# Performance work log

Measured on AMD Instinct MI355X. Metric: run time of the kernel, lower is better.

The kernel has to match this reference:

```python
import jax, jax.numpy as jnp
import numpy as np

INPUT_DIM = 256
EMBED_DIM = 256
NUM_HEADS = 8
HEAD_DIM = EMBED_DIM // NUM_HEADS
N_TOKENS = 11136
N_BATCH = 16


def _xavier(key, shape):
    fan_out, fan_in = shape
    bound = np.sqrt(6.0 / (fan_in + fan_out)).astype(np.float32)
    return jax.random.uniform(key, shape, jnp.float32, -bound, bound)


def setup_inputs() -> dict:
    key = jax.random.key(0)
    k_x, k_ids, k_qkv, k_o = jax.random.split(key, 4)
    x = jax.random.normal(k_x, (N_TOKENS, INPUT_DIM), jnp.float32)
    batch_ids = jnp.sort(jax.random.randint(k_ids, (N_TOKENS,), 0, N_BATCH)).astype(jnp.int32)
    qkv_w = _xavier(k_qkv, (3 * EMBED_DIM, INPUT_DIM))
    qkv_b = jnp.zeros((3 * EMBED_DIM,), jnp.float32)
    o_w = _xavier(k_o, (EMBED_DIM, EMBED_DIM))
    o_b = jnp.zeros((EMBED_DIM,), jnp.float32)
    return {"x": x, "batch_ids": batch_ids, "qkv_w": qkv_w, "qkv_b": qkv_b,
            "o_w": o_w, "o_b": o_b}


def reference(x, batch_ids, qkv_w, qkv_b, o_w, o_b):
    # batch_ids is concrete metadata (mirrors np.unique on CPU in the original).
    ids = np.asarray(batch_ids)
    vals, counts = np.unique(ids, return_counts=True)
    B = len(vals)
    S = int(counts.max())
    offsets = np.concatenate([np.zeros(1, np.int64), np.cumsum(counts)[:-1]])
    seg = np.searchsorted(vals, ids)               # segment index per token
    pos = np.arange(ids.shape[0]) - offsets[seg]   # position within segment

    qkv = x @ qkv_w.T + qkv_b                      # [N, 3E]
    # pad_sequence with padding_value=1 -> scatter tokens into an all-ones buffer
    fin = jnp.ones((B, S, 3 * EMBED_DIM), qkv.dtype).at[seg, pos].set(qkv)
    # padded rows sum to exactly 3E (all ones) -> mask True marks padding
    pad_mask = fin.sum(-1) >= fin.shape[-1]        # [B, S]

    qkv4 = fin.reshape(B, S, NUM_HEADS, 3 * HEAD_DIM).transpose(0, 2, 1, 3)
    q, k, v = jnp.split(qkv4, 3, axis=-1)          # each [B, H, S, hd]

    logits = jnp.einsum('bhqd,bhkd->bhqk', q, k) * (HEAD_DIM ** -0.5)
    logits = jnp.where(pad_mask[:, None, None, :], -jnp.inf, logits)
    attn = jax.nn.softmax(logits, axis=-1)         # [B, H, S, S]

    out = jnp.einsum('bhqk,bhkd->bhqd', attn, v)
    out = out.transpose(0, 2, 1, 3).reshape(B, S, EMBED_DIM)
    out = out[seg, pos]                            # unpad -> [N, E]
    return out @ o_w.T + o_b
```

## Files before the change

kernel.cpp:

```cpp
#include <hip/hip_runtime.h>
#include <stdint.h>


#define N_TOK 11136
#define E 256
#define H 8
#define HD 32

typedef __attribute__((ext_vector_type(8))) __bf16 bf16x8;
typedef __attribute__((ext_vector_type(8))) unsigned short u16x8;
typedef __attribute__((ext_vector_type(4))) float f32x4;

__device__ __forceinline__ unsigned short f2bf(float f) {
  unsigned int u = __float_as_uint(f);
  u = (u + 0x7FFFu + ((u >> 16) & 1u)) >> 16;
  return (unsigned short)u;
}
__device__ __forceinline__ float bf2f(unsigned short s) {
  return __uint_as_float(((unsigned int)s) << 16);
}
__device__ __forceinline__ bf16x8 ld8(const unsigned short* p) {
  return *(const bf16x8*)p;
}
__device__ __forceinline__ unsigned int cvtpk(float a, float b) {
  unsigned int r;
  asm("v_cvt_pk_bf16_f32 %0, %1, %2" : "=v"(r) : "v"(a), "v"(b));
  return r;
}

__global__ void k_split(const float* __restrict__ x, const float* __restrict__ qw,
                        const float* __restrict__ ow, const int* __restrict__ ids,
                        unsigned short* __restrict__ xhi, unsigned short* __restrict__ xlo,
                        unsigned short* __restrict__ whi, unsigned short* __restrict__ wlo,
                        unsigned short* __restrict__ owb, int* __restrict__ offs) {
  if (blockIdx.x == 0 && threadIdx.x < 17) {
    int b = threadIdx.x, lo = 0, hi = N_TOK;
    while (lo < hi) { int mid = (lo + hi) >> 1; if (ids[mid] < b) lo = mid + 1; else hi = mid; }
    offs[b] = lo;
  }
  const int NX4 = N_TOK * E / 4;
  const int NW4 = 3 * E * E / 4;
  const int NO4 = E * E / 4;
  int total = NX4 + NW4 + NO4;
  for (int i = blockIdx.x * blockDim.x + threadIdx.x; i < total;
       i += gridDim.x * blockDim.x) {
    if (i < NX4) {
      float4 v = ((const float4*)x)[i];
      ushort4 hv, lv;
      hv.x = f2bf(v.x); lv.x = f2bf(v.x - bf2f(hv.x));
      hv.y = f2bf(v.y); lv.y = f2bf(v.y - bf2f(hv.y));
      hv.z = f2bf(v.z); lv.z = f2bf(v.z - bf2f(hv.z));
      hv.w = f2bf(v.w); lv.w = f2bf(v.w - bf2f(hv.w));
      ((ushort4*)xhi)[i] = hv; ((ushort4*)xlo)[i] = lv;
    } else if (i < NX4 + NW4) {
      int j = i - NX4;
      float4 v = ((const float4*)qw)[j];
      ushort4 hv, lv;
      hv.x = f2bf(v.x); lv.x = f2bf(v.x - bf2f(hv.x));
      hv.y = f2bf(v.y); lv.y = f2bf(v.y - bf2f(hv.y));
      hv.z = f2bf(v.z); lv.z = f2bf(v.z - bf2f(hv.z));
      hv.w = f2bf(v.w); lv.w = f2bf(v.w - bf2f(hv.w));
      ((ushort4*)whi)[j] = hv; ((ushort4*)wlo)[j] = lv;
    } else {
      int j = i - NX4 - NW4;
      float4 v = ((const float4*)ow)[j];
      ushort4 hv;
      hv.x = f2bf(v.x); hv.y = f2bf(v.y); hv.z = f2bf(v.z); hv.w = f2bf(v.w);
      ((ushort4*)owb)[j] = hv;
    }
  }
}

#define QK_BSTRIDE 264
#define QSCALE (0.17677669529663687f * 1.4426950408889634f)
#define SQ_STR 36
#define SK_STR 20
__global__ __launch_bounds__(256, 3) void k_qkv(
    const unsigned short* __restrict__ xhi, const unsigned short* __restrict__ xlo,
    const unsigned short* __restrict__ whi, const unsigned short* __restrict__ wlo,
    const float* __restrict__ qkv_b,
    unsigned short* __restrict__ Qb, unsigned short* __restrict__ Kb,
    unsigned short* __restrict__ Vt) {
  int bid = blockIdx.x + 16 * blockIdx.y;
  int xcd = bid & 7;
  int j8 = bid >> 3;
  int colb = j8 & 15;
  int tile = (j8 >> 4) * 8 + xcd;
  if (tile >= 58) return;
  int col0 = colb * 48;
  __shared__ __align__(16) unsigned short Bhi[48 * QK_BSTRIDE];
  __shared__ __align__(16) unsigned short Blo[48 * QK_BSTRIDE];
  int tid = threadIdx.x;
  int w = tid >> 6, lane = tid & 63, m = lane & 15, quad = lane >> 4;
  int rowb = tile * 192 + w * 48;

  {
    const u16x8* wh8 = (const u16x8*)(whi + (size_t)col0 * E);
    const u16x8* wl8 = (const u16x8*)(wlo + (size_t)col0 * E);
#pragma unroll
    for (int i = 0; i < 6; ++i) {
      int flat = i * 256 + tid;
      int row = flat >> 5, c8 = flat & 31;
      *(u16x8*)(Bhi + row * QK_BSTRIDE + c8 * 8) = wh8[flat];
      *(u16x8*)(Blo + row * QK_BSTRIDE + c8 * 8) = wl8[flat];
    }
  }
  __syncthreads();

  f32x4 acc[3][3] = {};
  bf16x8 ah1[3], al1[3], ah2[3], al2[3];
#pragma unroll
  for (int mt = 0; mt < 3; ++mt) {
    const size_t ro = (size_t)(rowb + mt * 16 + m) * E + quad * 8;
    ah1[mt] = ld8(xhi + ro);       al1[mt] = ld8(xlo + ro);
    ah2[mt] = ld8(xhi + ro + 32);  al2[mt] = ld8(xlo + ro + 32);
  }
  for (int kc = 0; kc < 8; ++kc) {
    bf16x8 ah[3], al[3];
#pragma unroll
    for (int mt = 0; mt < 3; ++mt) {
      ah[mt] = ah1[mt]; al[mt] = al1[mt];
      ah1[mt] = ah2[mt]; al1[mt] = al2[mt];
    }
    int kn = kc + 2; if (kn > 7) kn = 7;
    int kon = kn * 32 + quad * 8;
#pragma unroll
    for (int mt = 0; mt < 3; ++mt) {
      const size_t ro = (size_t)(rowb + mt * 16 + m) * E + kon;
      ah2[mt] = ld8(xhi + ro);
      al2[mt] = ld8(xlo + ro);
    }
    int ko = kc * 32 + quad * 8;
#pragma unroll
    for (int t = 0; t < 3; ++t) {
      bf16x8 bh = ld8(Bhi + (16 * t + m) * QK_BSTRIDE + ko);
      bf16x8 bl = ld8(Blo + (16 * t + m) * QK_BSTRIDE + ko);
#pragma unroll
      for (int mt = 0; mt < 3; ++mt) {
        acc[mt][t] = __builtin_amdgcn_mfma_f32_16x16x32_bf16(ah[mt], bh, acc[mt][t], 0, 0, 0);
        acc[mt][t] = __builtin_amdgcn_mfma_f32_16x16x32_bf16(ah[mt], bl, acc[mt][t], 0, 0, 0);
        acc[mt][t] = __builtin_amdgcn_mfma_f32_16x16x32_bf16(al[mt], bh, acc[mt][t], 0, 0, 0);
      }
    }
  }
  __syncthreads();
  unsigned short* SQ = Bhi + w * (48 * SQ_STR);
  unsigned short* SK = Bhi + 4 * (48 * SQ_STR) + w * (48 * SK_STR);
  int evenb = !(colb & 1);
  int hd = col0 / 96;
  if (evenb) {
#pragma unroll
    for (int t = 0; t < 2; ++t) {
      float bias = qkv_b[col0 + 16 * t + m];
#pragma unroll
      for (int mt = 0; mt < 3; ++mt)
#pragma unroll
        for (int r = 0; r < 4; ++r) {
          int row = mt * 16 + quad * 4 + r;
          SQ[row * SQ_STR + 16 * t + m] = f2bf((acc[mt][t][r] + bias) * QSCALE);
        }
    }
    {
      float bias = qkv_b[col0 + 32 + m];
#pragma unroll
      for (int mt = 0; mt < 3; ++mt)
#pragma unroll
        for (int r = 0; r < 4; ++r) {
          int row = mt * 16 + quad * 4 + r;
          SK[row * SK_STR + m] = f2bf(acc[mt][2][r] + bias);
        }
    }
  } else {
    {
      float bias = qkv_b[col0 + m];
#pragma unroll
      for (int mt = 0; mt < 3; ++mt)
#pragma unroll
        for (int r = 0; r < 4; ++r) {
          int row = mt * 16 + quad * 4 + r;
          SK[row * SK_STR + m] = f2bf(acc[mt][0][r] + bias);
        }
    }
#pragma unroll
    for (int t = 1; t < 3; ++t) {
      int j = col0 + 16 * t + m;
      int hdv = j / 96;
      int rr = j - hdv * 96;
      int d = rr - 64;
      float bias = qkv_b[j];
#pragma unroll
      for (int mt = 0; mt < 3; ++mt) {
        int tokb = rowb + mt * 16 + quad * 4;
        ushort4 pk;
        pk.x = f2bf(acc[mt][t][0] + bias); pk.y = f2bf(acc[mt][t][1] + bias);
        pk.z = f2bf(acc[mt][t][2] + bias); pk.w = f2bf(acc[mt][t][3] + bias);
        *(ushort4*)(Vt + (size_t)(hdv * HD + d) * N_TOK + tokb) = pk;
      }
    }
  }
  asm volatile("s_waitcnt lgkmcnt(0)" ::: "memory");
  if (evenb) {
    int row16 = lane >> 2, chunk = lane & 3;
#pragma unroll
    for (int it = 0; it < 3; ++it) {
      int row = it * 16 + row16;
      int tok = rowb + row;
      bf16x8 v = ld8(SQ + row * SQ_STR + chunk * 8);
      *(bf16x8*)(Qb + ((size_t)hd * N_TOK + tok) * HD + chunk * 8) = v;
    }
  }
  {
    int kd0 = evenb ? 0 : 16;
    int row32 = lane >> 1, half = lane & 1;
#pragma unroll
    for (int it = 0; it < 2; ++it) {
      int row = it * 32 + row32;
      if (row < 48) {
        int tok = rowb + row;
        bf16x8 v = ld8(SK + row * SK_STR + half * 8);
        *(bf16x8*)(Kb + ((size_t)hd * N_TOK + tok) * HD + kd0 + half * 8) = v;
      }
    }
  }
}

#define PSTRIDE 72
#define VSTR 72
__global__ __launch_bounds__(512, 4) void k_attn(
    const int* __restrict__ ids, const int* __restrict__ offs,
    const unsigned short* __restrict__ Qb, const unsigned short* __restrict__ Kb,
    const unsigned short* __restrict__ Vt,
    unsigned short* __restrict__ attnb) {
  __shared__ __align__(16) unsigned short Kl[2][64 * 32];
  __shared__ __align__(16) unsigned short Vl[2][32 * VSTR];
  __shared__ __align__(16) unsigned short ldsP[8][16 * PSTRIDE];
  __shared__ int bred[16];
  int tid = threadIdx.x;
  int w = tid >> 6, lane = tid & 63;
  int m = lane & 15, quad = lane >> 4;
  int h = blockIdx.x;
  int tok0 = blockIdx.y * 128;
  int q0 = tok0 + w * 16;
  unsigned short* P = ldsP[w];
  int tok = q0 + m;
  int b = ids[tok];
  int st = offs[b], en = offs[b + 1];
  int kmin = st, kmax = en, stM = st, enm = en;
#pragma unroll
  for (int d = 1; d <= 8; d <<= 1) {
    kmin = min(kmin, __shfl_xor(kmin, d));
    kmax = max(kmax, __shfl_xor(kmax, d));
    stM  = max(stM,  __shfl_xor(stM,  d));
    enm  = min(enm,  __shfl_xor(enm,  d));
  }
  if (lane == 0) { bred[w] = kmin; bred[8 + w] = kmax; }

  const unsigned short* Kbase = Kb + (size_t)h * N_TOK * HD;
  const unsigned short* Vbase = Vt + (size_t)h * HD * N_TOK;
  bf16x8 qf = ld8(Qb + (size_t)(h * N_TOK + tok) * HD + quad * 8);

  bool isK = (tid < 256);
  int krow = tid >> 2, kgof = (tid & 3) * 8;
  int vt = tid - 256;
  int vrow = vt >> 3, vgof = (vt & 7) * 8;
  const unsigned short* gsrc = isK ? (Kbase + (size_t)krow * HD + kgof)
                                   : (Vbase + (size_t)vrow * N_TOK + vgof);
  size_t gmul = isK ? HD : 1;
  int ldsoff = isK ? (krow * 32 + kgof) : (vrow * VSTR + vgof);

  __syncthreads();
  int kminB = bred[0], kmaxB = bred[8];
#pragma unroll
  for (int i = 1; i < 8; ++i) {
    kminB = min(kminB, bred[i]);
    kmaxB = max(kmaxB, bred[8 + i]);
  }
  int k0beg = kminB & ~63;

  bf16x8 g = ld8(gsrc + (size_t)k0beg * gmul);
  *(bf16x8*)((isK ? &Kl[0][0] : &Vl[0][0]) + ldsoff) = g;
  __syncthreads();

  float lsum = 0.f;
  f32x4 o0 = {}, o1 = {};
  int buf = 0;
  for (int k0 = k0beg; k0 < kmaxB; k0 += 64) {
    int k1 = (k0 + 64 < kmaxB) ? (k0 + 64) : k0;
    g = ld8(gsrc + (size_t)k1 * gmul);
    const unsigned short* Kc = &Kl[buf][0];
    const unsigned short* Vc = &Vl[buf][0];
    f32x4 s[4];
    __builtin_amdgcn_s_setprio(1);
#pragma unroll
    for (int i = 0; i < 4; ++i) {
      bf16x8 kf = ld8(Kc + (16 * i + m) * 32 + quad * 8);
      f32x4 z = {};
      s[i] = __builtin_amdgcn_mfma_f32_16x16x32_bf16(kf, qf, z, 0, 0, 0);
    }
    __builtin_amdgcn_s_setprio(0);
    bool interior = (k0 >= stM && k0 + 64 <= enm);
    int jb = k0 + quad * 4;
#pragma unroll
    for (int i = 0; i < 4; ++i) {
      float p[4];
#pragma unroll
      for (int r = 0; r < 4; ++r) {
        float sv = s[i][r];
        if (!interior) {
          int j = jb + 16 * i + r;
          sv = (j >= st && j < en) ? sv : -3e38f;
        }
        float e;
        asm("v_exp_f32 %0, %1" : "=v"(e) : "v"(sv));
        p[r] = e;
      }
      lsum += (p[0] + p[1]) + (p[2] + p[3]);
      uint2 pk;
      pk.x = cvtpk(p[0], p[1]);
      pk.y = cvtpk(p[2], p[3]);
      *(uint2*)(P + m * PSTRIDE + 16 * i + quad * 4) = pk;
    }
    __builtin_amdgcn_s_setprio(1);
#pragma unroll
    for (int c = 0; c < 2; ++c) {
      bf16x8 pf  = ld8(P + m * PSTRIDE + 32 * c + quad * 8);
      bf16x8 vf0 = ld8(Vc + m * VSTR + 32 * c + quad * 8);
      bf16x8 vf1 = ld8(Vc + (16 + m) * VSTR + 32 * c + quad * 8);
      o0 = __builtin_amdgcn_mfma_f32_16x16x32_bf16(vf0, pf, o0, 0, 0, 0);
      o1 = __builtin_amdgcn_mfma_f32_16x16x32_bf16(vf1, pf, o1, 0, 0, 0);
    }
    __builtin_amdgcn_s_setprio(0);
    *(bf16x8*)((isK ? &Kl[buf ^ 1][0] : &Vl[buf ^ 1][0]) + ldsoff) = g;
    __syncthreads();
    buf ^= 1;
  }
  lsum += __shfl_xor(lsum, 16);
  lsum += __shfl_xor(lsum, 32);
  float inv = 1.0f / lsum;
  uint2 w0, w1;
  w0.x = cvtpk(o0[0] * inv, o0[1] * inv);
  w0.y = cvtpk(o0[2] * inv, o0[3] * inv);
  w1.x = cvtpk(o1[0] * inv, o1[1] * inv);
  w1.y = cvtpk(o1[2] * inv, o1[3] * inv);
  *(uint2*)(attnb + (size_t)tok * E + h * HD + quad * 4) = w0;
  *(uint2*)(attnb + (size_t)tok * E + h * HD + 16 + quad * 4) = w1;
}

__global__ __launch_bounds__(256, 4) void k_oproj(
    const unsigned short* __restrict__ attnb, const unsigned short* __restrict__ owb,
    const float* __restrict__ ob, float* __restrict__ out) {
  __shared__ __align__(16) unsigned short Bo[64 * QK_BSTRIDE];
  int tid = threadIdx.x;
  int w = tid >> 6, lane = tid & 63, m = lane & 15, quad = lane >> 4;
  int tok0 = blockIdx.x * 64, col0 = blockIdx.y * 64;
  {
    const u16x8* o8 = (const u16x8*)(owb + (size_t)col0 * E);
#pragma unroll
    for (int i = 0; i < 8; ++i) {
      int flat = i * 256 + tid;
      int row = flat >> 5, c8 = flat & 31;
      *(u16x8*)(Bo + row * QK_BSTRIDE + c8 * 8) = o8[flat];
    }
  }
  __syncthreads();
  f32x4 acc[4] = {};
  int arow = tok0 + 16 * w + m;
  const unsigned short* abase = attnb + (size_t)arow * E + quad * 8;
  bf16x8 a1 = ld8(abase);
  bf16x8 a2 = ld8(abase + 32);
  for (int kc = 0; kc < 8; ++kc) {
    bf16x8 a = a1;
    a1 = a2;
    int kn = kc + 2; if (kn > 7) kn = 7;
    a2 = ld8(abase + kn * 32);
    int ko = kc * 32 + quad * 8;
#pragma unroll
    for (int t = 0; t < 4; ++t) {
      bf16x8 b = ld8(Bo + (16 * t + m) * QK_BSTRIDE + ko);
      acc[t] = __builtin_amdgcn_mfma_f32_16x16x32_bf16(a, b, acc[t], 0, 0, 0);
    }
  }
#pragma unroll
  for (int t = 0; t < 4; ++t) {
    int j = col0 + 16 * t + m;
    float bias = ob[j];
#pragma unroll
    for (int r = 0; r < 4; ++r) {
      int tok = tok0 + 16 * w + quad * 4 + r;
      out[(size_t)tok * E + j] = acc[t][r] + bias;
    }
  }
}

extern "C" void kernel_launch(void* const* d_in, const int* in_sizes, int n_in,
                              void* d_out, int out_size, void* d_ws, size_t ws_size,
                              hipStream_t stream) {
  const float* x   = (const float*)d_in[0];
  const int*   ids = (const int*)d_in[1];
  const float* qw  = (const float*)d_in[2];
  const float* qb  = (const float*)d_in[3];
  const float* ow  = (const float*)d_in[4];
  const float* ob  = (const float*)d_in[5];
  float* out = (float*)d_out;

  char* p = (char*)d_ws;
  auto alloc = [&](size_t bytes) {
    char* r = p;
    p += (bytes + 255) & ~(size_t)255;
    return r;
  };
  int* offs = (int*)alloc(32 * sizeof(int));
  unsigned short* xhi = (unsigned short*)alloc((size_t)N_TOK * E * 2);
  unsigned short* xlo = (unsigned short*)alloc((size_t)N_TOK * E * 2);
  unsigned short* whi = (unsigned short*)alloc((size_t)3 * E * E * 2);
  unsigned short* wlo = (unsigned short*)alloc((size_t)3 * E * E * 2);
  unsigned short* owb = (unsigned short*)alloc((size_t)E * E * 2);
  unsigned short* Qb  = (unsigned short*)alloc((size_t)N_TOK * E * 2);
  unsigned short* Kb  = (unsigned short*)alloc((size_t)N_TOK * E * 2);
  unsigned short* Vt  = (unsigned short*)alloc((size_t)N_TOK * E * 2);
  unsigned short* att = (unsigned short*)alloc((size_t)N_TOK * E * 2);

  k_split<<<dim3(1712), dim3(256), 0, stream>>>(x, qw, ow, ids, xhi, xlo, whi, wlo, owb, offs);
  k_qkv<<<dim3(16, 64), dim3(256), 0, stream>>>(xhi, xlo, whi, wlo, qb, Qb, Kb, Vt);
  k_attn<<<dim3(H, N_TOK / 128), dim3(512), 0, stream>>>(ids, offs, Qb, Kb, Vt, att);
  k_oproj<<<dim3(N_TOK / 64, E / 64), dim3(256), 0, stream>>>(att, owb, ob, out);
}
```

Measured before the change: 152.0 us.

## Fuse fp32-to-bf16 hi/lo split into QKV and output projection kernels

Removes the separate split kernel and converts x, the QKV weights and the output weights from fp32 to bf16 hi/lo pairs on the fly inside the GEMM kernels. Segment offset computation moves into the first QKV block. This drops one launch and the round trip of writing and re-reading bf16 copies. The cost is more conversion ALU work in the GEMMs, since weights are reconverted per block and x is loaded as fp32, which is twice the bytes of a bf16 copy. It also adds register pressure from holding fp32 prefetch buffers.

```diff
diff --git a/kernel.cpp b/kernel.cpp
--- a/kernel.cpp
+++ b/kernel.cpp
@@ -27,48 +27,18 @@
   asm("v_cvt_pk_bf16_f32 %0, %1, %2" : "=v"(r) : "v"(a), "v"(b));
   return r;
 }
-
-__global__ void k_split(const float* __restrict__ x, const float* __restrict__ qw,
-                        const float* __restrict__ ow, const int* __restrict__ ids,
-                        unsigned short* __restrict__ xhi, unsigned short* __restrict__ xlo,
-                        unsigned short* __restrict__ whi, unsigned short* __restrict__ wlo,
-                        unsigned short* __restrict__ owb, int* __restrict__ offs) {
-  if (blockIdx.x == 0 && threadIdx.x < 17) {
-    int b = threadIdx.x, lo = 0, hi = N_TOK;
-    while (lo < hi) { int mid = (lo + hi) >> 1; if (ids[mid] < b) lo = mid + 1; else hi = mid; }
-    offs[b] = lo;
-  }
-  const int NX4 = N_TOK * E / 4;
-  const int NW4 = 3 * E * E / 4;
-  const int NO4 = E * E / 4;
-  int total = NX4 + NW4 + NO4;
-  for (int i = blockIdx.x * blockDim.x + threadIdx.x; i < total;
-       i += gridDim.x * blockDim.x) {
-    if (i < NX4) {
-      float4 v = ((const float4*)x)[i];
-      ushort4 hv, lv;
-      hv.x = f2bf(v.x); lv.x = f2bf(v.x - bf2f(hv.x));
-      hv.y = f2bf(v.y); lv.y = f2bf(v.y - bf2f(hv.y));
-      hv.z = f2bf(v.z); lv.z = f2bf(v.z - bf2f(hv.z));
-      hv.w = f2bf(v.w); lv.w = f2bf(v.w - bf2f(hv.w));
-      ((ushort4*)xhi)[i] = hv; ((ushort4*)xlo)[i] = lv;
-    } else if (i < NX4 + NW4) {
-      int j = i - NX4;
-      float4 v = ((const float4*)qw)[j];
-      ushort4 hv, lv;
-      hv.x = f2bf(v.x); lv.x = f2bf(v.x - bf2f(hv.x));
-      hv.y = f2bf(v.y); lv.y = f2bf(v.y - bf2f(hv.y));
-      hv.z = f2bf(v.z); lv.z = f2bf(v.z - bf2f(hv.z));
-      hv.w = f2bf(v.w); lv.w = f2bf(v.w - bf2f(hv.w));
-      ((ushort4*)whi)[j] = hv; ((ushort4*)wlo)[j] = lv;
-    } else {
-      int j = i - NX4 - NW4;
-      float4 v = ((const float4*)ow)[j];
-      ushort4 hv;
-      hv.x = f2bf(v.x); hv.y = f2bf(v.y); hv.z = f2bf(v.z); hv.w = f2bf(v.w);
-      ((ushort4*)owb)[j] = hv;
-    }
-  }
+__device__ __forceinline__ void f32_hilo8(const float4 a, const float4 b,
+                                          bf16x8* hp, bf16x8* lp) {
+  u16x8 h, l;
+  const float ff[8] = {a.x, a.y, a.z, a.w, b.x, b.y, b.z, b.w};
+#pragma unroll
+  for (int j = 0; j < 8; ++j) {
+    unsigned short hh = f2bf(ff[j]);
+    h[j] = hh;
+    l[j] = f2bf(ff[j] - bf2f(hh));
+  }
+  *hp = *(bf16x8*)&h;
+  *lp = *(bf16x8*)&l;
 }
 
 #define QK_BSTRIDE 264
@@ -76,11 +46,15 @@
 #define SQ_STR 36
 #define SK_STR 20
 __global__ __launch_bounds__(256, 3) void k_qkv(
-    const unsigned short* __restrict__ xhi, const unsigned short* __restrict__ xlo,
-    const unsigned short* __restrict__ whi, const unsigned short* __restrict__ wlo,
-    const float* __restrict__ qkv_b,
+    const float* __restrict__ x, const float* __restrict__ qw,
+    const float* __restrict__ qkv_b, const int* __restrict__ ids,
     unsigned short* __restrict__ Qb, unsigned short* __restrict__ Kb,
-    unsigned short* __restrict__ Vt) {
+    unsigned short* __restrict__ Vt, int* __restrict__ offs) {
+  if (blockIdx.x == 0 && blockIdx.y == 0 && threadIdx.x < 17) {
+    int b = threadIdx.x, lo = 0, hi = N_TOK;
+    while (lo < hi) { int mid = (lo + hi) >> 1; if (ids[mid] < b) lo = mid + 1; else hi = mid; }
+    offs[b] = lo;
+  }
   int bid = blockIdx.x + 16 * blockIdx.y;
   int xcd = bid & 7;
   int j8 = bid >> 3;
@@ -95,40 +69,42 @@
   int rowb = tile * 192 + w * 48;
 
   {
-    const u16x8* wh8 = (const u16x8*)(whi + (size_t)col0 * E);
-    const u16x8* wl8 = (const u16x8*)(wlo + (size_t)col0 * E);
+    const float* wsrc = qw + (size_t)col0 * E;
 #pragma unroll
     for (int i = 0; i < 6; ++i) {
       int flat = i * 256 + tid;
       int row = flat >> 5, c8 = flat & 31;
-      *(u16x8*)(Bhi + row * QK_BSTRIDE + c8 * 8) = wh8[flat];
-      *(u16x8*)(Blo + row * QK_BSTRIDE + c8 * 8) = wl8[flat];
+      const float* pp = wsrc + row * E + c8 * 8;
+      float4 a = *(const float4*)pp, b = *(const float4*)(pp + 4);
+      bf16x8 hv, lv;
+      f32_hilo8(a, b, &hv, &lv);
+      *(bf16x8*)(Bhi + row * QK_BSTRIDE + c8 * 8) = hv;
+      *(bf16x8*)(Blo + row * QK_BSTRIDE + c8 * 8) = lv;
     }
   }
   __syncthreads();
 
   f32x4 acc[3][3] = {};
-  bf16x8 ah1[3], al1[3], ah2[3], al2[3];
+  float4 xa[3][2], xb[3][2];
 #pragma unroll
   for (int mt = 0; mt < 3; ++mt) {
-    const size_t ro = (size_t)(rowb + mt * 16 + m) * E + quad * 8;
-    ah1[mt] = ld8(xhi + ro);       al1[mt] = ld8(xlo + ro);
-    ah2[mt] = ld8(xhi + ro + 32);  al2[mt] = ld8(xlo + ro + 32);
+    const float* rp = x + (size_t)(rowb + mt * 16 + m) * E + quad * 8;
+    xa[mt][0] = *(const float4*)rp;        xa[mt][1] = *(const float4*)(rp + 4);
+    xb[mt][0] = *(const float4*)(rp + 32); xb[mt][1] = *(const float4*)(rp + 36);
   }
   for (int kc = 0; kc < 8; ++kc) {
     bf16x8 ah[3], al[3];
 #pragma unroll
     for (int mt = 0; mt < 3; ++mt) {
-      ah[mt] = ah1[mt]; al[mt] = al1[mt];
-      ah1[mt] = ah2[mt]; al1[mt] = al2[mt];
+      f32_hilo8(xa[mt][0], xa[mt][1], &ah[mt], &al[mt]);
+      xa[mt][0] = xb[mt][0]; xa[mt][1] = xb[mt][1];
     }
     int kn = kc + 2; if (kn > 7) kn = 7;
-    int kon = kn * 32 + quad * 8;
 #pragma unroll
     for (int mt = 0; mt < 3; ++mt) {
-      const size_t ro = (size_t)(rowb + mt * 16 + m) * E + kon;
-      ah2[mt] = ld8(xhi + ro);
-      al2[mt] = ld8(xlo + ro);
+      const float* rp = x + (size_t)(rowb + mt * 16 + m) * E + kn * 32 + quad * 8;
+      xb[mt][0] = *(const float4*)rp;
+      xb[mt][1] = *(const float4*)(rp + 4);
     }
     int ko = kc * 32 + quad * 8;
 #pragma unroll
@@ -347,19 +323,24 @@
 }
 
 __global__ __launch_bounds__(256, 4) void k_oproj(
-    const unsigned short* __restrict__ attnb, const unsigned short* __restrict__ owb,
+    const unsigned short* __restrict__ attnb, const float* __restrict__ ow,
     const float* __restrict__ ob, float* __restrict__ out) {
   __shared__ __align__(16) unsigned short Bo[64 * QK_BSTRIDE];
   int tid = threadIdx.x;
   int w = tid >> 6, lane = tid & 63, m = lane & 15, quad = lane >> 4;
   int tok0 = blockIdx.x * 64, col0 = blockIdx.y * 64;
   {
-    const u16x8* o8 = (const u16x8*)(owb + (size_t)col0 * E);
+    const float* osrc = ow + (size_t)col0 * E;
 #pragma unroll
     for (int i = 0; i < 8; ++i) {
       int flat = i * 256 + tid;
       int row = flat >> 5, c8 = flat & 31;
-      *(u16x8*)(Bo + row * QK_BSTRIDE + c8 * 8) = o8[flat];
+      const float* pp = osrc + row * E + c8 * 8;
+      float4 a = *(const float4*)pp, b = *(const float4*)(pp + 4);
+      u16x8 hv;
+      hv[0] = f2bf(a.x); hv[1] = f2bf(a.y); hv[2] = f2bf(a.z); hv[3] = f2bf(a.w);
+      hv[4] = f2bf(b.x); hv[5] = f2bf(b.y); hv[6] = f2bf(b.z); hv[7] = f2bf(b.w);
+      *(u16x8*)(Bo + row * QK_BSTRIDE + c8 * 8) = hv;
     }
   }
   __syncthreads();
@@ -410,18 +391,12 @@
     return r;
   };
   int* offs = (int*)alloc(32 * sizeof(int));
-  unsigned short* xhi = (unsigned short*)alloc((size_t)N_TOK * E * 2);
-  unsigned short* xlo = (unsigned short*)alloc((size_t)N_TOK * E * 2);
-  unsigned short* whi = (unsigned short*)alloc((size_t)3 * E * E * 2);
-  unsigned short* wlo = (unsigned short*)alloc((size_t)3 * E * E * 2);
-  unsigned short* owb = (unsigned short*)alloc((size_t)E * E * 2);
   unsigned short* Qb  = (unsigned short*)alloc((size_t)N_TOK * E * 2);
   unsigned short* Kb  = (unsigned short*)alloc((size_t)N_TOK * E * 2);
   unsigned short* Vt  = (unsigned short*)alloc((size_t)N_TOK * E * 2);
   unsigned short* att = (unsigned short*)alloc((size_t)N_TOK * E * 2);
 
-  k_split<<<dim3(1712), dim3(256), 0, stream>>>(x, qw, ow, ids, xhi, xlo, whi, wlo, owb, offs);
-  k_qkv<<<dim3(16, 64), dim3(256), 0, stream>>>(xhi, xlo, whi, wlo, qb, Qb, Kb, Vt);
+  k_qkv<<<dim3(16, 64), dim3(256), 0, stream>>>(x, qw, qb, ids, Qb, Kb, Vt, offs);
   k_attn<<<dim3(H, N_TOK / 128), dim3(512), 0, stream>>>(ids, offs, Qb, Kb, Vt, att);
-  k_oproj<<<dim3(N_TOK / 64, E / 64), dim3(256), 0, stream>>>(att, owb, ob, out);
-}
+  k_oproj<<<dim3(N_TOK / 64, E / 64), dim3(256), 0, stream>>>(att, ow, ob, out);
+}
```

Result: slower. 236.1 us (+55.3%).
